# Performance work log

Hardware: AMD Instinct MI355X
Metric: run time of the kernel (lower is better)

Reference implementation:

```python
import jax, jax.numpy as jnp
import numpy as np

B, T, E = 2, 4096, 768
N_HEADS = 12
HEAD_DIM = E // N_HEADS


def setup_inputs() -> dict:
    key = jax.random.key(0)
    k1, k2, k3 = jax.random.split(key, 3)
    x = jax.random.normal(k1, (B, T, E), dtype=jnp.float32)
    W_attn = jax.random.normal(k2, (E, 3 * E), dtype=jnp.float32) * (1.0 / np.sqrt(E))
    b_attn = jnp.zeros((3 * E,), dtype=jnp.float32)
    W_proj = jax.random.normal(k3, (E, E), dtype=jnp.float32) * (1.0 / np.sqrt(E))
    b_proj = jnp.zeros((E,), dtype=jnp.float32)
    return {"x": x, "W_attn": W_attn, "b_attn": b_attn, "W_proj": W_proj, "b_proj": b_proj}


def reference(x, W_attn, b_attn, W_proj, b_proj):
    Bx, Tx, Ex = x.shape
    qkv = x @ W_attn + b_attn                      # [B,T,3E]
    q, k, v = jnp.split(qkv, 3, axis=-1)
    # [B,T,E] -> [B,H,T,D]
    def to_heads(t):
        return t.reshape(Bx, Tx, N_HEADS, HEAD_DIM).transpose(0, 2, 1, 3)
    q, k, v = to_heads(q), to_heads(k), to_heads(v)
    scale = 1.0 / np.sqrt(HEAD_DIM).astype(np.float32)
    scores = jnp.einsum('bhqd,bhkd->bhqk', q, k) * scale  # [B,H,T,T]
    causal = jnp.tril(jnp.ones((Tx, Tx), dtype=bool))
    scores = jnp.where(causal[None, None, :, :], scores, -jnp.inf)
    probs = jax.nn.softmax(scores, axis=-1)
    y = jnp.einsum('bhqk,bhkd->bhqd', probs, v)    # [B,H,T,D]
    y = y.transpose(0, 2, 1, 3).reshape(Bx, Tx, Ex)
    return y @ W_proj + b_proj
```

## Files before the change

kernel.cpp:

```cpp
#include <hip/hip_runtime.h>


#define SEQT 4096
#define EMB  768
#define NHEAD 12
#define HDIM 64

typedef __attribute__((ext_vector_type(8))) short bf16x8;
typedef __attribute__((ext_vector_type(4))) float f32x4;

static __device__ __forceinline__ unsigned short f2bf(float f) {
  union { float f; unsigned u; } a; a.f = f;
  unsigned u = a.u;
  u += 0x7FFF + ((u >> 16) & 1);
  return (unsigned short)(u >> 16);
}

__global__ __launch_bounds__(256) void cast_bf16_kernel(
    const float* __restrict__ in, short* __restrict__ out, int n4) {
  int i = blockIdx.x * 256 + threadIdx.x;
  if (i >= n4) return;
  float4 v = ((const float4*)in)[i];
  ushort4 o;
  o.x = f2bf(v.x); o.y = f2bf(v.y); o.z = f2bf(v.z); o.w = f2bf(v.w);
  ((ushort4*)out)[i] = o;
}

__global__ __launch_bounds__(256) void transpose_bf16_kernel(
    const float* __restrict__ in, short* __restrict__ out, int R, int C) {
  __shared__ float tile[32][33];
  int c0 = blockIdx.x * 32, r0 = blockIdx.y * 32;
  int tx = threadIdx.x, ty = threadIdx.y;
#pragma unroll
  for (int j = 0; j < 32; j += 8)
    tile[ty + j][tx] = in[(size_t)(r0 + ty + j) * C + (c0 + tx)];
  __syncthreads();
#pragma unroll
  for (int j = 0; j < 32; j += 8)
    out[(size_t)(c0 + ty + j) * R + (r0 + tx)] = (short)f2bf(tile[tx][ty + j]);
}

#define GP 40
template <int MODE>
__global__ __launch_bounds__(256) void gemm_kernel(
    const short* __restrict__ A, const short* __restrict__ Bt,
    const float* __restrict__ bias, int K,
    short* __restrict__ Qg, short* __restrict__ Kg, short* __restrict__ Vtg,
    float* __restrict__ Out, int Ncols) {
  __shared__ short As[64 * GP];
  __shared__ short Bs[64 * GP];
  int tid = threadIdx.x;
  int w = tid >> 6, l = tid & 63, quad = l >> 4, lo = l & 15;
  int gm = blockIdx.x, gn = blockIdx.y;
  f32x4 acc[4] = {};
  int ra = tid >> 2, cq = tid & 3;
  const short* Aptr = A + (size_t)(gm * 64 + ra) * K + cq * 8;
  const short* Bptr = Bt + (size_t)(gn * 64 + ra) * K + cq * 8;

  for (int kk = 0; kk < K; kk += 32) {
    uint4 av = *(const uint4*)(Aptr + kk);
    uint4 bv = *(const uint4*)(Bptr + kk);
    *(uint4*)&As[ra * GP + cq * 8] = av;
    *(uint4*)&Bs[ra * GP + cq * 8] = bv;
    __syncthreads();
    bf16x8 bfr = *(const bf16x8*)&Bs[(w * 16 + lo) * GP + quad * 8];
#pragma unroll
    for (int mt = 0; mt < 4; mt++) {
      bf16x8 afr = *(const bf16x8*)&As[(mt * 16 + lo) * GP + quad * 8];
      acc[mt] = __builtin_amdgcn_mfma_f32_16x16x32_bf16(afr, bfr, acc[mt], 0, 0, 0);
    }
    __syncthreads();
  }

  int n = gn * 64 + w * 16 + lo;
  float bias_v = bias[n];
#pragma unroll
  for (int mt = 0; mt < 4; mt++) {
#pragma unroll
    for (int r = 0; r < 4; r++) {
      int m = gm * 64 + mt * 16 + quad * 4 + r;
      float v = acc[mt][r] + bias_v;
      if (MODE == 0) {
        int b = m >> 12, t = m & 4095;
        if (n < EMB) {
          int h = n >> 6, d = n & 63;
          Qg[(((size_t)b * NHEAD + h) * SEQT + t) * HDIM + d] = (short)f2bf(v);
        } else if (n < 2 * EMB) {
          int n2 = n - EMB, h = n2 >> 6, d = n2 & 63;
          Kg[(((size_t)b * NHEAD + h) * SEQT + t) * HDIM + d] = (short)f2bf(v);
        } else {
          int n2 = n - 2 * EMB, h = n2 >> 6, d = n2 & 63;
          Vtg[(((size_t)b * NHEAD + h) * HDIM + d) * SEQT + t] = (short)f2bf(v);
        }
      } else {
        Out[(size_t)m * Ncols + n] = v;
      }
    }
  }
}

#define AP 72
__global__ __launch_bounds__(256, 3) void attn_kernel(
    const short* __restrict__ Qg, const short* __restrict__ Kg,
    const short* __restrict__ Vtg, short* __restrict__ Y) {
  __shared__ short Ks[64 * AP];
  __shared__ short Vs[64 * AP];
  __shared__ short Ps[4][32 * AP];
  int tid = threadIdx.x;
  int w = tid >> 6, l = tid & 63, quad = l >> 4, lo = l & 15;
  int bh = blockIdx.x;
  int y = blockIdx.y;
  int qt = (y & 1) ? (31 - (y >> 1)) : (y >> 1);
  int q0 = qt * 128;
  int b = bh / NHEAD, h = bh % NHEAD;
  const short* Qbase = Qg + (size_t)bh * SEQT * HDIM;
  const short* Kbase = Kg + (size_t)bh * SEQT * HDIM;
  const short* Vbase = Vtg + (size_t)bh * HDIM * SEQT;
  short* Pw = &Ps[w][0];

  int qw = q0 + w * 32;
  bf16x8 qf[2][2];
#pragma unroll
  for (int s = 0; s < 2; s++) {
    const short* qp = &Qbase[(size_t)(qw + s * 16 + lo) * HDIM + quad * 8];
    qf[s][0] = *(const bf16x8*)qp;
    qf[s][1] = *(const bf16x8*)(qp + 32);
  }

  f32x4 O[2][4] = {};
  float m_s[2] = {-1e30f, -1e30f};
  float l_s[2] = {0.f, 0.f};

  int sr = tid >> 2, sc = tid & 3;
  const float SC = 0.18033688011112042f;

  int nkv = q0 + 128;
  for (int kv0 = 0; kv0 < nkv; kv0 += 64) {
    const short* kg = &Kbase[(size_t)(kv0 + sr) * HDIM];
    const short* vg = &Vbase[(size_t)sr * SEQT + kv0];
    uint4 k0 = *(const uint4*)(kg + sc * 8);
    uint4 k1 = *(const uint4*)(kg + sc * 8 + 32);
    uint4 v0 = *(const uint4*)(vg + sc * 8);
    uint4 v1 = *(const uint4*)(vg + sc * 8 + 32);
    *(uint4*)&Ks[sr * AP + sc * 8] = k0;
    *(uint4*)&Ks[sr * AP + sc * 8 + 32] = k1;
    *(uint4*)&Vs[sr * AP + sc * 8] = v0;
    *(uint4*)&Vs[sr * AP + sc * 8 + 32] = v1;
    __syncthreads();

    f32x4 st[2][4] = {};
#pragma unroll
    for (int t = 0; t < 4; t++) {
      const short* kp = &Ks[(t * 16 + lo) * AP + quad * 8];
      bf16x8 ka = *(const bf16x8*)kp;
      bf16x8 kb2 = *(const bf16x8*)(kp + 32);
      st[0][t] = __builtin_amdgcn_mfma_f32_16x16x32_bf16(ka,  qf[0][0], st[0][t], 0, 0, 0);
      st[0][t] = __builtin_amdgcn_mfma_f32_16x16x32_bf16(kb2, qf[0][1], st[0][t], 0, 0, 0);
      st[1][t] = __builtin_amdgcn_mfma_f32_16x16x32_bf16(ka,  qf[1][0], st[1][t], 0, 0, 0);
      st[1][t] = __builtin_amdgcn_mfma_f32_16x16x32_bf16(kb2, qf[1][1], st[1][t], 0, 0, 0);
    }

#pragma unroll
    for (int s = 0; s < 2; s++) {
      int qs = qw + s * 16;
      float mx = -1e30f;
#pragma unroll
      for (int t = 0; t < 4; t++) {
        int kb = kv0 + t * 16;
        if (kb < qs) {
#pragma unroll
          for (int r = 0; r < 4; r++) {
            st[s][t][r] *= SC;
            mx = fmaxf(mx, st[s][t][r]);
          }
        } else if (kb == qs) {
#pragma unroll
          for (int r = 0; r < 4; r++) {
            st[s][t][r] = (quad * 4 + r <= lo) ? st[s][t][r] * SC : -1e30f;
            mx = fmaxf(mx, st[s][t][r]);
          }
        } else {
#pragma unroll
          for (int r = 0; r < 4; r++) st[s][t][r] = -1e30f;
        }
      }
      mx = fmaxf(mx, __shfl_xor(mx, 16));
      mx = fmaxf(mx, __shfl_xor(mx, 32));
      float mn = fmaxf(m_s[s], mx);
      float al = __builtin_amdgcn_exp2f(m_s[s] - mn);
      m_s[s] = mn;
      float sm = 0.f;
#pragma unroll
      for (int t = 0; t < 4; t++) {
        int kb = kv0 + t * 16;
        ushort4 pk;
        if (kb <= qs) {
          float p0 = __builtin_amdgcn_exp2f(st[s][t][0] - mn);
          float p1 = __builtin_amdgcn_exp2f(st[s][t][1] - mn);
          float p2 = __builtin_amdgcn_exp2f(st[s][t][2] - mn);
          float p3 = __builtin_amdgcn_exp2f(st[s][t][3] - mn);
          sm += (p0 + p1) + (p2 + p3);
          pk.x = f2bf(p0); pk.y = f2bf(p1); pk.z = f2bf(p2); pk.w = f2bf(p3);
        } else {
          pk.x = 0; pk.y = 0; pk.z = 0; pk.w = 0;
        }
        *(ushort4*)&Pw[(s * 16 + lo) * AP + t * 16 + quad * 4] = pk;
      }
      sm += __shfl_xor(sm, 16);
      sm += __shfl_xor(sm, 32);
      l_s[s] = l_s[s] * al + sm;
#pragma unroll
      for (int dt = 0; dt < 4; dt++)
#pragma unroll
        for (int r = 0; r < 4; r++) O[s][dt][r] *= al;
    }

    bf16x8 pfr[2][2];
#pragma unroll
    for (int s = 0; s < 2; s++) {
      const short* pp = &Pw[(s * 16 + lo) * AP + quad * 8];
      pfr[s][0] = *(const bf16x8*)pp;
      pfr[s][1] = *(const bf16x8*)(pp + 32);
    }
#pragma unroll
    for (int dt = 0; dt < 4; dt++) {
      const short* vp = &Vs[(dt * 16 + lo) * AP + quad * 8];
      bf16x8 va = *(const bf16x8*)vp;
      bf16x8 vb = *(const bf16x8*)(vp + 32);
#pragma unroll
      for (int s = 0; s < 2; s++) {
        O[s][dt] = __builtin_amdgcn_mfma_f32_16x16x32_bf16(va, pfr[s][0], O[s][dt], 0, 0, 0);
        O[s][dt] = __builtin_amdgcn_mfma_f32_16x16x32_bf16(vb, pfr[s][1], O[s][dt], 0, 0, 0);
      }
    }
    __syncthreads();
  }

#pragma unroll
  for (int s = 0; s < 2; s++) {
    float rl = 1.f / l_s[s];
    int q = qw + s * 16 + lo;
    short* yp = &Y[((size_t)b * SEQT + q) * EMB + h * 64 + quad * 4];
#pragma unroll
    for (int dt = 0; dt < 4; dt++) {
      ushort4 o;
      o.x = f2bf(O[s][dt][0] * rl);
      o.y = f2bf(O[s][dt][1] * rl);
      o.z = f2bf(O[s][dt][2] * rl);
      o.w = f2bf(O[s][dt][3] * rl);
      *(ushort4*)(yp + dt * 16) = o;
    }
  }
}

extern "C" void kernel_launch(void* const* d_in, const int* in_sizes, int n_in,
                              void* d_out, int out_size, void* d_ws, size_t ws_size,
                              hipStream_t stream) {
  const float* x      = (const float*)d_in[0];
  const float* W_attn = (const float*)d_in[1];
  const float* b_attn = (const float*)d_in[2];
  const float* W_proj = (const float*)d_in[3];
  const float* b_proj = (const float*)d_in[4];
  float* out = (float*)d_out;

  char* ws = (char*)d_ws;
  short* x_bf = (short*)(ws + 0);
  short* Wt_a = (short*)(ws + 12582912);
  short* Wt_p = (short*)(ws + 16121856);
  short* Qg   = (short*)(ws + 17301504);
  short* Kg   = (short*)(ws + 29884416);
  short* Vtg  = (short*)(ws + 42467328);
  short* Ybf  = (short*)(ws + 55050240);

  cast_bf16_kernel<<<6144, 256, 0, stream>>>(x, x_bf, 1572864);
  transpose_bf16_kernel<<<dim3(72, 24), dim3(32, 8), 0, stream>>>(W_attn, Wt_a, 768, 2304);
  transpose_bf16_kernel<<<dim3(24, 24), dim3(32, 8), 0, stream>>>(W_proj, Wt_p, 768, 768);

  gemm_kernel<0><<<dim3(128, 36), 256, 0, stream>>>(x_bf, Wt_a, b_attn, 768,
                                                    Qg, Kg, Vtg, nullptr, 0);
  attn_kernel<<<dim3(24, 32), 256, 0, stream>>>(Qg, Kg, Vtg, Ybf);
  gemm_kernel<1><<<dim3(128, 12), 256, 0, stream>>>(Ybf, Wt_p, b_proj, 768,
                                                    nullptr, nullptr, nullptr, out, 768);
}
```

Before: 322.0 us.

## Rewrite GEMMs with 128x128 tiles and attention with 32x32 MFMA register softmax

The GEMMs move to 128x128 block tiles where each wave computes a 64x64 sub-tile, and they stage operands with direct global-to-LDS loads. The attention kernel switches to 32x32x16 MFMA over 256-row query tiles and keeps probabilities in registers, exchanging halves across lanes instead of round-tripping through LDS. It also skips fully masked KV sub-tiles, orders blocks heaviest-first, and folds the scale into an FMA. The aim is more data reuse per load and less LDS traffic. The cost is higher register pressure, lower occupancy (launch bounds 2), and fewer blocks for load balancing.

Result: slower. 334.4 us (+3.9%).

```diff
diff --git a/kernel.cpp b/kernel.cpp
--- a/kernel.cpp
+++ b/kernel.cpp
@@ -8,12 +8,24 @@
 
 typedef __attribute__((ext_vector_type(8))) short bf16x8;
 typedef __attribute__((ext_vector_type(4))) float f32x4;
+typedef __attribute__((ext_vector_type(16))) float f32x16;
 
 static __device__ __forceinline__ unsigned short f2bf(float f) {
   union { float f; unsigned u; } a; a.f = f;
   unsigned u = a.u;
   u += 0x7FFF + ((u >> 16) & 1);
   return (unsigned short)(u >> 16);
+}
+
+static __device__ __forceinline__ unsigned pack_bf16(float a, float b) {
+  union { float f; unsigned u; } ua, ub; ua.f = a; ub.f = b;
+  return __builtin_amdgcn_perm(ub.u + 0x8000u, ua.u + 0x8000u, 0x07060302u);
+}
+
+static __device__ __forceinline__ void gload_lds16(const short* g, short* l) {
+  __builtin_amdgcn_global_load_lds(
+      (const __attribute__((address_space(1))) unsigned*)(const void*)g,
+      (__attribute__((address_space(3))) unsigned*)(void*)l, 16, 0, 0);
 }
 
 __global__ __launch_bounds__(256) void cast_bf16_kernel(
@@ -40,197 +52,239 @@
     out[(size_t)(c0 + ty + j) * R + (r0 + tx)] = (short)f2bf(tile[tx][ty + j]);
 }
 
-#define GP 40
 template <int MODE>
-__global__ __launch_bounds__(256) void gemm_kernel(
+__global__ __launch_bounds__(256) void gemm128_kernel(
     const short* __restrict__ A, const short* __restrict__ Bt,
     const float* __restrict__ bias, int K,
     short* __restrict__ Qg, short* __restrict__ Kg, short* __restrict__ Vtg,
-    float* __restrict__ Out, int Ncols) {
-  __shared__ short As[64 * GP];
-  __shared__ short Bs[64 * GP];
+    float* __restrict__ Out) {
+  __shared__ short As[128 * 32];
+  __shared__ short Bs[128 * 32];
   int tid = threadIdx.x;
   int w = tid >> 6, l = tid & 63, quad = l >> 4, lo = l & 15;
+  int wm = (w >> 1) * 64, wn = (w & 1) * 64;
   int gm = blockIdx.x, gn = blockIdx.y;
-  f32x4 acc[4] = {};
-  int ra = tid >> 2, cq = tid & 3;
-  const short* Aptr = A + (size_t)(gm * 64 + ra) * K + cq * 8;
-  const short* Bptr = Bt + (size_t)(gn * 64 + ra) * K + cq * 8;
+  f32x4 acc[4][4] = {};
+  int c0 = tid, c1 = tid + 256;
+  const short* Ag0 = A + (size_t)(gm * 128 + (c0 >> 2)) * K + (c0 & 3) * 8;
+  const short* Ag1 = A + (size_t)(gm * 128 + (c1 >> 2)) * K + (c1 & 3) * 8;
+  const short* Bg0 = Bt + (size_t)(gn * 128 + (c0 >> 2)) * K + (c0 & 3) * 8;
+  const short* Bg1 = Bt + (size_t)(gn * 128 + (c1 >> 2)) * K + (c1 & 3) * 8;
 
   for (int kk = 0; kk < K; kk += 32) {
-    uint4 av = *(const uint4*)(Aptr + kk);
-    uint4 bv = *(const uint4*)(Bptr + kk);
-    *(uint4*)&As[ra * GP + cq * 8] = av;
-    *(uint4*)&Bs[ra * GP + cq * 8] = bv;
+    gload_lds16(Ag0 + kk, &As[c0 * 8]);
+    gload_lds16(Ag1 + kk, &As[c1 * 8]);
+    gload_lds16(Bg0 + kk, &Bs[c0 * 8]);
+    gload_lds16(Bg1 + kk, &Bs[c1 * 8]);
     __syncthreads();
-    bf16x8 bfr = *(const bf16x8*)&Bs[(w * 16 + lo) * GP + quad * 8];
-#pragma unroll
-    for (int mt = 0; mt < 4; mt++) {
-      bf16x8 afr = *(const bf16x8*)&As[(mt * 16 + lo) * GP + quad * 8];
-      acc[mt] = __builtin_amdgcn_mfma_f32_16x16x32_bf16(afr, bfr, acc[mt], 0, 0, 0);
-    }
+    bf16x8 af[4], bf[4];
+#pragma unroll
+    for (int mt = 0; mt < 4; mt++)
+      af[mt] = *(const bf16x8*)&As[(wm + mt * 16 + lo) * 32 + quad * 8];
+#pragma unroll
+    for (int nt = 0; nt < 4; nt++)
+      bf[nt] = *(const bf16x8*)&Bs[(wn + nt * 16 + lo) * 32 + quad * 8];
+#pragma unroll
+    for (int mt = 0; mt < 4; mt++)
+#pragma unroll
+      for (int nt = 0; nt < 4; nt++)
+        acc[mt][nt] = __builtin_amdgcn_mfma_f32_16x16x32_bf16(af[mt], bf[nt], acc[mt][nt], 0, 0, 0);
     __syncthreads();
   }
 
-  int n = gn * 64 + w * 16 + lo;
-  float bias_v = bias[n];
-#pragma unroll
-  for (int mt = 0; mt < 4; mt++) {
-#pragma unroll
-    for (int r = 0; r < 4; r++) {
-      int m = gm * 64 + mt * 16 + quad * 4 + r;
-      float v = acc[mt][r] + bias_v;
-      if (MODE == 0) {
-        int b = m >> 12, t = m & 4095;
-        if (n < EMB) {
-          int h = n >> 6, d = n & 63;
-          Qg[(((size_t)b * NHEAD + h) * SEQT + t) * HDIM + d] = (short)f2bf(v);
-        } else if (n < 2 * EMB) {
-          int n2 = n - EMB, h = n2 >> 6, d = n2 & 63;
-          Kg[(((size_t)b * NHEAD + h) * SEQT + t) * HDIM + d] = (short)f2bf(v);
+#pragma unroll
+  for (int nt = 0; nt < 4; nt++) {
+    int n = gn * 128 + wn + nt * 16 + lo;
+    float bias_v = bias[n];
+#pragma unroll
+    for (int mt = 0; mt < 4; mt++) {
+#pragma unroll
+      for (int r = 0; r < 4; r++) {
+        int m = gm * 128 + wm + mt * 16 + quad * 4 + r;
+        float v = acc[mt][nt][r] + bias_v;
+        if (MODE == 0) {
+          int b = m >> 12, t = m & 4095;
+          if (n < EMB) {
+            int h = n >> 6, d = n & 63;
+            Qg[(((size_t)b * NHEAD + h) * SEQT + t) * HDIM + d] = (short)f2bf(v);
+          } else if (n < 2 * EMB) {
+            int n2 = n - EMB, h = n2 >> 6, d = n2 & 63;
+            Kg[(((size_t)b * NHEAD + h) * SEQT + t) * HDIM + d] = (short)f2bf(v);
+          } else {
+            int n2 = n - 2 * EMB, h = n2 >> 6, d = n2 & 63;
+            Vtg[(((size_t)b * NHEAD + h) * HDIM + d) * SEQT + t] = (short)f2bf(v);
+          }
         } else {
-          int n2 = n - 2 * EMB, h = n2 >> 6, d = n2 & 63;
-          Vtg[(((size_t)b * NHEAD + h) * HDIM + d) * SEQT + t] = (short)f2bf(v);
-        }
-      } else {
-        Out[(size_t)m * Ncols + n] = v;
+          Out[(size_t)m * EMB + n] = v;
+        }
       }
     }
   }
 }
 
 #define AP 72
-__global__ __launch_bounds__(256, 3) void attn_kernel(
+#define NEG_BIG (-1e9f)
+__global__ __launch_bounds__(256, 2) void attn_kernel(
     const short* __restrict__ Qg, const short* __restrict__ Kg,
     const short* __restrict__ Vtg, short* __restrict__ Y) {
   __shared__ short Ks[64 * AP];
   __shared__ short Vs[64 * AP];
-  __shared__ short Ps[4][32 * AP];
   int tid = threadIdx.x;
-  int w = tid >> 6, l = tid & 63, quad = l >> 4, lo = l & 15;
-  int bh = blockIdx.x;
-  int y = blockIdx.y;
-  int qt = (y & 1) ? (31 - (y >> 1)) : (y >> 1);
-  int q0 = qt * 128;
+  int w = tid >> 6, l = tid & 63;
+  int li = l & 31, hi = l >> 5;
+  int bid = blockIdx.x;
+  int qt = 15 - bid / 24;
+  int bh = bid % 24;
+  int q0 = qt * 256;
   int b = bh / NHEAD, h = bh % NHEAD;
   const short* Qbase = Qg + (size_t)bh * SEQT * HDIM;
   const short* Kbase = Kg + (size_t)bh * SEQT * HDIM;
   const short* Vbase = Vtg + (size_t)bh * HDIM * SEQT;
-  short* Pw = &Ps[w][0];
-
-  int qw = q0 + w * 32;
-  bf16x8 qf[2][2];
-#pragma unroll
-  for (int s = 0; s < 2; s++) {
-    const short* qp = &Qbase[(size_t)(qw + s * 16 + lo) * HDIM + quad * 8];
-    qf[s][0] = *(const bf16x8*)qp;
-    qf[s][1] = *(const bf16x8*)(qp + 32);
-  }
-
-  f32x4 O[2][4] = {};
-  float m_s[2] = {-1e30f, -1e30f};
+
+  int qw = q0 + w * 64;
+  bf16x8 qf[2][4];
+#pragma unroll
+  for (int s = 0; s < 2; s++)
+#pragma unroll
+    for (int kk = 0; kk < 4; kk++)
+      qf[s][kk] = *(const bf16x8*)&Qbase[(size_t)(qw + s * 32 + li) * HDIM + kk * 16 + hi * 8];
+
+  f32x16 O[2][2] = {};
+  float m_s[2] = {NEG_BIG, NEG_BIG};
   float l_s[2] = {0.f, 0.f};
 
   int sr = tid >> 2, sc = tid & 3;
   const float SC = 0.18033688011112042f;
-
-  int nkv = q0 + 128;
+  int qe = qw + 64;
+  int nkv = q0 + 256;
+
   for (int kv0 = 0; kv0 < nkv; kv0 += 64) {
-    const short* kg = &Kbase[(size_t)(kv0 + sr) * HDIM];
-    const short* vg = &Vbase[(size_t)sr * SEQT + kv0];
-    uint4 k0 = *(const uint4*)(kg + sc * 8);
-    uint4 k1 = *(const uint4*)(kg + sc * 8 + 32);
-    uint4 v0 = *(const uint4*)(vg + sc * 8);
-    uint4 v1 = *(const uint4*)(vg + sc * 8 + 32);
+    const short* kg = &Kbase[(size_t)(kv0 + sr) * HDIM + sc * 8];
+    const short* vg = &Vbase[(size_t)sr * SEQT + kv0 + sc * 8];
+    uint4 k0 = *(const uint4*)kg;
+    uint4 k1 = *(const uint4*)(kg + 32);
+    uint4 v0 = *(const uint4*)vg;
+    uint4 v1 = *(const uint4*)(vg + 32);
     *(uint4*)&Ks[sr * AP + sc * 8] = k0;
     *(uint4*)&Ks[sr * AP + sc * 8 + 32] = k1;
     *(uint4*)&Vs[sr * AP + sc * 8] = v0;
     *(uint4*)&Vs[sr * AP + sc * 8 + 32] = v1;
     __syncthreads();
 
-    f32x4 st[2][4] = {};
-#pragma unroll
-    for (int t = 0; t < 4; t++) {
-      const short* kp = &Ks[(t * 16 + lo) * AP + quad * 8];
-      bf16x8 ka = *(const bf16x8*)kp;
-      bf16x8 kb2 = *(const bf16x8*)(kp + 32);
-      st[0][t] = __builtin_amdgcn_mfma_f32_16x16x32_bf16(ka,  qf[0][0], st[0][t], 0, 0, 0);
-      st[0][t] = __builtin_amdgcn_mfma_f32_16x16x32_bf16(kb2, qf[0][1], st[0][t], 0, 0, 0);
-      st[1][t] = __builtin_amdgcn_mfma_f32_16x16x32_bf16(ka,  qf[1][0], st[1][t], 0, 0, 0);
-      st[1][t] = __builtin_amdgcn_mfma_f32_16x16x32_bf16(kb2, qf[1][1], st[1][t], 0, 0, 0);
-    }
-
-#pragma unroll
-    for (int s = 0; s < 2; s++) {
-      int qs = qw + s * 16;
-      float mx = -1e30f;
-#pragma unroll
-      for (int t = 0; t < 4; t++) {
-        int kb = kv0 + t * 16;
-        if (kb < qs) {
-#pragma unroll
-          for (int r = 0; r < 4; r++) {
-            st[s][t][r] *= SC;
-            mx = fmaxf(mx, st[s][t][r]);
-          }
-        } else if (kb == qs) {
-#pragma unroll
-          for (int r = 0; r < 4; r++) {
-            st[s][t][r] = (quad * 4 + r <= lo) ? st[s][t][r] * SC : -1e30f;
-            mx = fmaxf(mx, st[s][t][r]);
-          }
+    if (kv0 < qe) {
+      bf16x8 ka[2][4];
+#pragma unroll
+      for (int t = 0; t < 2; t++)
+#pragma unroll
+        for (int kk = 0; kk < 4; kk++)
+          ka[t][kk] = *(const bf16x8*)&Ks[(t * 32 + li) * AP + kk * 16 + hi * 8];
+
+      f32x16 st[2][2];
+#pragma unroll
+      for (int s = 0; s < 2; s++) {
+        int qbs = qw + s * 32;
+#pragma unroll
+        for (int t = 0; t < 2; t++) {
+          if (kv0 + t * 32 <= qbs + 31) {
+            f32x16 a = {};
+#pragma unroll
+            for (int kk = 0; kk < 4; kk++)
+              a = __builtin_amdgcn_mfma_f32_32x32x16_bf16(ka[t][kk], qf[s][kk], a, 0, 0, 0);
+            st[s][t] = a;
+          }
+        }
+      }
+
+      bf16x8 va[2][4];
+#pragma unroll
+      for (int dt = 0; dt < 2; dt++)
+#pragma unroll
+        for (int g = 0; g < 4; g++)
+          va[dt][g] = *(const bf16x8*)&Vs[(dt * 32 + li) * AP + g * 16 + hi * 8];
+
+#pragma unroll
+      for (int s = 0; s < 2; s++) {
+        int qbs = qw + s * 32;
+        if (kv0 > qbs + 31) continue;
+        bool full0 = (kv0 + 31 <= qbs);
+        bool act1 = (kv0 + 32 <= qbs + 31);
+        bool full1 = (kv0 + 63 <= qbs);
+        float mx = NEG_BIG;
+        if (full0) {
+#pragma unroll
+          for (int r = 0; r < 16; r++) mx = fmaxf(mx, st[s][0][r]);
         } else {
-#pragma unroll
-          for (int r = 0; r < 4; r++) st[s][t][r] = -1e30f;
-        }
-      }
-      mx = fmaxf(mx, __shfl_xor(mx, 16));
-      mx = fmaxf(mx, __shfl_xor(mx, 32));
-      float mn = fmaxf(m_s[s], mx);
-      float al = __builtin_amdgcn_exp2f(m_s[s] - mn);
-      m_s[s] = mn;
-      float sm = 0.f;
-#pragma unroll
-      for (int t = 0; t < 4; t++) {
-        int kb = kv0 + t * 16;
-        ushort4 pk;
-        if (kb <= qs) {
-          float p0 = __builtin_amdgcn_exp2f(st[s][t][0] - mn);
-          float p1 = __builtin_amdgcn_exp2f(st[s][t][1] - mn);
-          float p2 = __builtin_amdgcn_exp2f(st[s][t][2] - mn);
-          float p3 = __builtin_amdgcn_exp2f(st[s][t][3] - mn);
-          sm += (p0 + p1) + (p2 + p3);
-          pk.x = f2bf(p0); pk.y = f2bf(p1); pk.z = f2bf(p2); pk.w = f2bf(p3);
-        } else {
-          pk.x = 0; pk.y = 0; pk.z = 0; pk.w = 0;
-        }
-        *(ushort4*)&Pw[(s * 16 + lo) * AP + t * 16 + quad * 4] = pk;
-      }
-      sm += __shfl_xor(sm, 16);
-      sm += __shfl_xor(sm, 32);
-      l_s[s] = l_s[s] * al + sm;
-#pragma unroll
-      for (int dt = 0; dt < 4; dt++)
-#pragma unroll
-        for (int r = 0; r < 4; r++) O[s][dt][r] *= al;
-    }
-
-    bf16x8 pfr[2][2];
-#pragma unroll
-    for (int s = 0; s < 2; s++) {
-      const short* pp = &Pw[(s * 16 + lo) * AP + quad * 8];
-      pfr[s][0] = *(const bf16x8*)pp;
-      pfr[s][1] = *(const bf16x8*)(pp + 32);
-    }
-#pragma unroll
-    for (int dt = 0; dt < 4; dt++) {
-      const short* vp = &Vs[(dt * 16 + lo) * AP + quad * 8];
-      bf16x8 va = *(const bf16x8*)vp;
-      bf16x8 vb = *(const bf16x8*)(vp + 32);
-#pragma unroll
-      for (int s = 0; s < 2; s++) {
-        O[s][dt] = __builtin_amdgcn_mfma_f32_16x16x32_bf16(va, pfr[s][0], O[s][dt], 0, 0, 0);
-        O[s][dt] = __builtin_amdgcn_mfma_f32_16x16x32_bf16(vb, pfr[s][1], O[s][dt], 0, 0, 0);
+          int thr = qbs - kv0 + li - 4 * hi;
+#pragma unroll
+          for (int r = 0; r < 16; r++) {
+            const int R = (r & 3) + 8 * (r >> 2);
+            st[s][0][r] = (R <= thr) ? st[s][0][r] : NEG_BIG;
+            mx = fmaxf(mx, st[s][0][r]);
+          }
+        }
+        if (act1) {
+          if (full1) {
+#pragma unroll
+            for (int r = 0; r < 16; r++) mx = fmaxf(mx, st[s][1][r]);
+          } else {
+            int thr = qbs - kv0 - 32 + li - 4 * hi;
+#pragma unroll
+            for (int r = 0; r < 16; r++) {
+              const int R = (r & 3) + 8 * (r >> 2);
+              st[s][1][r] = (R <= thr) ? st[s][1][r] : NEG_BIG;
+              mx = fmaxf(mx, st[s][1][r]);
+            }
+          }
+        }
+        mx = fmaxf(mx, __shfl_xor(mx, 32));
+        float mn = fmaxf(m_s[s], mx);
+        float c1 = SC * mn;
+        float al = __builtin_amdgcn_exp2f(fminf(SC * m_s[s] - c1, 0.f));
+        m_s[s] = mn;
+        float sm = 0.f;
+        unsigned pk[2][8];
+#pragma unroll
+        for (int r2 = 0; r2 < 8; r2++) {
+          float pa = __builtin_amdgcn_exp2f(fminf(__builtin_fmaf(st[s][0][2 * r2],     SC, -c1), 0.f));
+          float pb = __builtin_amdgcn_exp2f(fminf(__builtin_fmaf(st[s][0][2 * r2 + 1], SC, -c1), 0.f));
+          sm += pa + pb;
+          pk[0][r2] = pack_bf16(pa, pb);
+        }
+        if (act1) {
+#pragma unroll
+          for (int r2 = 0; r2 < 8; r2++) {
+            float pa = __builtin_amdgcn_exp2f(fminf(__builtin_fmaf(st[s][1][2 * r2],     SC, -c1), 0.f));
+            float pb = __builtin_amdgcn_exp2f(fminf(__builtin_fmaf(st[s][1][2 * r2 + 1], SC, -c1), 0.f));
+            sm += pa + pb;
+            pk[1][r2] = pack_bf16(pa, pb);
+          }
+        }
+        sm += __shfl_xor(sm, 32);
+        l_s[s] = l_s[s] * al + sm;
+#pragma unroll
+        for (int dt = 0; dt < 2; dt++)
+#pragma unroll
+          for (int r = 0; r < 16; r++) O[s][dt][r] *= al;
+
+#pragma unroll
+        for (int g = 0; g < 4; g++) {
+          int t = g >> 1, k2 = g & 1;
+          if (t == 1 && !act1) continue;
+          unsigned own_a = hi ? pk[t][k2 * 4 + 2] : pk[t][k2 * 4 + 0];
+          unsigned own_b = hi ? pk[t][k2 * 4 + 3] : pk[t][k2 * 4 + 1];
+          unsigned snd_a = hi ? pk[t][k2 * 4 + 0] : pk[t][k2 * 4 + 2];
+          unsigned snd_b = hi ? pk[t][k2 * 4 + 1] : pk[t][k2 * 4 + 3];
+          unsigned rcv_a = (unsigned)__shfl_xor((int)snd_a, 32);
+          unsigned rcv_b = (unsigned)__shfl_xor((int)snd_b, 32);
+          union { unsigned u[4]; bf16x8 v; } pf;
+          pf.u[0] = hi ? rcv_a : own_a;
+          pf.u[1] = hi ? rcv_b : own_b;
+          pf.u[2] = hi ? own_a : rcv_a;
+          pf.u[3] = hi ? own_b : rcv_b;
+#pragma unroll
+          for (int dt = 0; dt < 2; dt++)
+            O[s][dt] = __builtin_amdgcn_mfma_f32_32x32x16_bf16(va[dt][g], pf.v, O[s][dt], 0, 0, 0);
+        }
       }
     }
     __syncthreads();
@@ -239,16 +293,17 @@
 #pragma unroll
   for (int s = 0; s < 2; s++) {
     float rl = 1.f / l_s[s];
-    int q = qw + s * 16 + lo;
-    short* yp = &Y[((size_t)b * SEQT + q) * EMB + h * 64 + quad * 4];
-#pragma unroll
-    for (int dt = 0; dt < 4; dt++) {
-      ushort4 o;
-      o.x = f2bf(O[s][dt][0] * rl);
-      o.y = f2bf(O[s][dt][1] * rl);
-      o.z = f2bf(O[s][dt][2] * rl);
-      o.w = f2bf(O[s][dt][3] * rl);
-      *(ushort4*)(yp + dt * 16) = o;
+    int q = qw + s * 32 + li;
+    short* yp = &Y[((size_t)b * SEQT + q) * EMB + h * 64];
+#pragma unroll
+    for (int dt = 0; dt < 2; dt++) {
+#pragma unroll
+      for (int rg = 0; rg < 4; rg++) {
+        uint2 u2;
+        u2.x = pack_bf16(O[s][dt][rg * 4 + 0] * rl, O[s][dt][rg * 4 + 1] * rl);
+        u2.y = pack_bf16(O[s][dt][rg * 4 + 2] * rl, O[s][dt][rg * 4 + 3] * rl);
+        *(uint2*)(yp + dt * 32 + rg * 8 + hi * 4) = u2;
+      }
     }
   }
 }
@@ -276,9 +331,9 @@
   transpose_bf16_kernel<<<dim3(72, 24), dim3(32, 8), 0, stream>>>(W_attn, Wt_a, 768, 2304);
   transpose_bf16_kernel<<<dim3(24, 24), dim3(32, 8), 0, stream>>>(W_proj, Wt_p, 768, 768);
 
-  gemm_kernel<0><<<dim3(128, 36), 256, 0, stream>>>(x_bf, Wt_a, b_attn, 768,
-                                                    Qg, Kg, Vtg, nullptr, 0);
-  attn_kernel<<<dim3(24, 32), 256, 0, stream>>>(Qg, Kg, Vtg, Ybf);
-  gemm_kernel<1><<<dim3(128, 12), 256, 0, stream>>>(Ybf, Wt_p, b_proj, 768,
-                                                    nullptr, nullptr, nullptr, out, 768);
-}
+  gemm128_kernel<0><<<dim3(64, 18), 256, 0, stream>>>(x_bf, Wt_a, b_attn, 768,
+                                                      Qg, Kg, Vtg, nullptr);
+  attn_kernel<<<384, 256, 0, stream>>>(Qg, Kg, Vtg, Ybf);
+  gemm128_kernel<1><<<dim3(64, 6), 256, 0, stream>>>(Ybf, Wt_p, b_proj, 768,
+                                                     nullptr, nullptr, nullptr, out);
+}
```
